# Optimization experiments

Measured on AMD Instinct MI355X. Metric: run time of the kernel, lower is better.

## Reference

```python
import jax, jax.numpy as jnp
import numpy as np

B, T = 256, 128
DW = 768          # dim_word
DH = 768          # dim_hidden (must equal DW per broadcast in original code)
NC = 3            # num_classification
VOCAB = 50000
TVOCAB = 5000


def setup_inputs() -> dict:
    key = jax.random.key(0)
    ks = jax.random.split(key, 16)
    u = 1.0 / np.sqrt(DH)
    uni = lambda k, shape: jax.random.uniform(k, shape, jnp.float32, -u, u)
    inp = {
        'sent': jax.random.randint(ks[0], (B, T), 0, VOCAB),
        'target': jax.random.randint(ks[1], (B,), 0, TVOCAB),
        'lens': jnp.clip(jax.random.randint(ks[2], (B,), 0, T + 1), 1, T),
        'emb': jax.random.normal(ks[3], (VOCAB, DW), jnp.float32) * 0.1,
        'temb': jax.random.normal(ks[4], (TVOCAB, DW), jnp.float32) * 0.1,
        # LSTM cell params: input = cat(x_t, target_x) -> 2*DW
        'W_ih': uni(ks[5], (2 * DW, 4 * DH)),
        'W_hh': uni(ks[6], (DH, 4 * DH)),
        'b_lstm': uni(ks[7], (4 * DH,)),
        'Wh': uni(ks[8], (DH, DH)),
        'Wv': uni(ks[9], (DW, DW)),
        'w': uni(ks[10], (DH + DW,)),
        'Wp': uni(ks[11], (DH, DH)),
        'Wx': uni(ks[12], (DH, DH)),
        'W_lin': uni(ks[13], (DH, NC)),
        'b_lin': uni(ks[14], (NC,)),
    }
    return inp


def _forward(sent, target, lens, emb, temb, W_ih, W_hh, b_lstm, Wh, Wv, w, Wp, Wx, W_lin, b_lin):
    x = emb[sent]                      # [B, T, DW]
    tx = temb[target]                  # [B, DW]
    mask = (jnp.arange(T)[None, :] < lens[:, None]).astype(x.dtype)  # [B, T]

    def step(carry, ins):
        h, c = carry
        xt, mt = ins                   # [B, DW], [B]
        inp = jnp.concatenate([xt, tx], axis=-1)          # [B, 2*DW]
        gates = inp @ W_ih + h @ W_hh + b_lstm            # [B, 4*DH]
        i, f, g, o = jnp.split(gates, 4, axis=-1)
        c_new = jax.nn.sigmoid(f) * c + jax.nn.sigmoid(i) * jnp.tanh(g)
        h_new = jax.nn.sigmoid(o) * jnp.tanh(c_new)
        m = mt[:, None]
        h = m * h_new + (1.0 - m) * h   # mask blend (hold state past seq end)
        c = m * c_new + (1.0 - m) * c
        return (h, c), h

    h0 = jnp.zeros((x.shape[0], DH), x.dtype)
    c0 = jnp.zeros((x.shape[0], DH), x.dtype)
    xs = (jnp.swapaxes(x, 0, 1), mask.T)                 # time-major
    _, Hs = jax.lax.scan(step, (h0, c0), xs)
    H = jnp.swapaxes(Hs, 0, 1)                            # [B, T, DH]

    # attention: M = tanh([H Wh ; aspect Wv]); scores = M @ w, masked softmax
    aspect_proj = (tx @ Wv)[:, None, :]                   # [B, 1, DW] broadcast over T
    M = jnp.tanh(jnp.concatenate(
        [H @ Wh, jnp.broadcast_to(aspect_proj, H.shape)], axis=-1))  # [B, T, DH+DW]
    scores = M @ w                                        # [B, T]
    scores = jnp.where(mask > 0, scores, -1e9)
    alpha = jax.nn.softmax(scores, axis=-1)               # [B, T]
    r = jnp.einsum('bt,btd->bd', alpha, H)                # [B, DH]
    h_star = jnp.tanh(r @ Wp + H[:, -1, :] @ Wx)          # [B, DH]
    # dropout is identity in eval mode
    logit = h_star @ W_lin + b_lin                        # [B, NC]
    return logit


def reference(sent, target, lens, emb, temb, W_ih, W_hh, b_lstm, Wh, Wv, w, Wp, Wx, W_lin, b_lin):
    return _forward(sent, target, lens, emb, temb, W_ih, W_hh, b_lstm,
                    Wh, Wv, w, Wp, Wx, W_lin, b_lin)
```

## Files before the change

kernel.cpp:

```cpp
#include <hip/hip_runtime.h>
#include <stdint.h>

#define Bz 256
#define Tz 128
#define DWz 768
#define DHz 768
#define G4z 3072
#define NBLK 96
#define NGRID 256

typedef __attribute__((ext_vector_type(8))) short short8;
typedef __attribute__((ext_vector_type(4))) float f32x4;
typedef __attribute__((ext_vector_type(4))) int i32x4;

__device__ __forceinline__ unsigned short f2bf(float x) {
    union { float f; unsigned int u; } v; v.f = x;
    unsigned int u = v.u;
    return (unsigned short)((u + 0x7fffu + ((u >> 16) & 1u)) >> 16);
}
__device__ __forceinline__ float bf2f(unsigned short h) {
    union { unsigned int u; float f; } v; v.u = ((unsigned int)h) << 16;
    return v.f;
}
__device__ __forceinline__ float fsigm(float x) {
// ... 175 lines not shown
    int s0 = tid, s1 = tid + 256;
    int bd0 = (s0 >> 2) * 40 + (((s0 & 3) ^ (((s0 >> 2) >> 3) & 3)) << 3);
    int bd1 = (s1 >> 2) * 40 + (((s1 & 3) ^ (((s1 >> 2) >> 3) & 3)) << 3);

    f32x4 acc[4][4];
    f32x4 zz = {0.f, 0.f, 0.f, 0.f};
#pragma unroll
    for (int i = 0; i < 4; ++i)
#pragma unroll
        for (int j = 0; j < 4; ++j) acc[i][j] = zz;

    for (int k0 = 0; k0 < DWz; k0 += 32) {
        {
            const float* src = emb + gbase + k0 + kp;
            alignas(16) unsigned short tmp[16];
#pragma unroll
            for (int it = 0; it < 4; ++it) {
                float4 v = ((const float4*)src)[it];
                tmp[it * 4 + 0] = f2bf(v.x); tmp[it * 4 + 1] = f2bf(v.y);
                tmp[it * 4 + 2] = f2bf(v.z); tmp[it * 4 + 3] = f2bf(v.w);
            }
            *(int4*)(sA + arow * 40 + kp) = *(const int4*)tmp;
            *(int4*)(sA + arow * 40 + kp + 8) = *(const int4*)(tmp + 8);
        }
        {
            const int4* wsrc = (const int4*)WbP
                + ((long)((k0 >> 5) * 24 + (n0 >> 7))) * 512 + tid;
            int4 v0 = wsrc[0];
            int4 v1 = wsrc[256];
            *(int4*)(sB + bd0) = v0;
            *(int4*)(sB + bd1) = v1;
        }
        __syncthreads();
        short8 af[4], bfr[4];
#pragma unroll
        for (int i = 0; i < 4; ++i)
            af[i] = *(const short8*)(sA + (wm * 64 + i * 16 + l15) * 40 + q * 8);
#pragma unroll
        for (int j = 0; j < 4; ++j) {
            int n = wn * 64 + j * 16 + l15;
            bfr[j] = *(const short8*)(sB + n * 40 + ((q ^ ((n >> 3) & 3)) << 3));
        }
#pragma unroll
        for (int i = 0; i < 4; ++i)
#pragma unroll
            for (int j = 0; j < 4; ++j)
                acc[i][j] = __builtin_amdgcn_mfma_f32_16x16x32_bf16(af[i], bfr[j], acc[i][j], 0, 0, 0);
        __syncthreads();
    }
#pragma unroll
    for (int j = 0; j < 4; ++j) {
        int n = n0 + wn * 64 + j * 16 + l15;
        int gt = n / 768;
        int dblk = (n - gt * 768) >> 4;
#pragma unroll
        for (int ip = 0; ip < 2; ++ip) {
            int row = m0 + wm * 64 + ip * 32;
            int t = row >> 8;
            int bq = (row & 255) + q * 4;
            int blk = dblk * 2 + (bq >> 7);
            int tidd = ((bq & 127) >> 5) * 64 + q * 16 + l15;
            alignas(16) unsigned short o[8];
#pragma unroll
            for (int r = 0; r < 4; ++r) {
                o[r]     = f2bf(acc[ip * 2][j][r]);
                o[4 + r] = f2bf(acc[ip * 2 + 1][j][r]);
            }
            *(int4*)(xW + (((long)t * 96 + blk) * 4 + gt) * 2048 + (long)tidd * 8) = *(const int4*)o;
        }
    }
}

#define UNPACK(PF, G)                                                        \
    {                                                                        \
        const unsigned short* ch_ = (const unsigned short*)&(PF);            \
        _Pragma("unroll")                                                    \
        for (int i_ = 0; i_ < 2; ++i_)                                       \
            _Pragma("unroll")                                                \
            for (int r_ = 0; r_ < 4; ++r_)                                   \
                xg[i_][G][r_] = bf2f(ch_[i_ * 4 + r_]) + xgc[i_][G][r_];     \
    }

__global__ __launch_bounds__(256, 1) void k_lstm_all(int t0, int t1,
        unsigned short* __restrict__ xW, const float* __restrict__ constg,
        const unsigned short* __restrict__ WhhP, unsigned short* __restrict__ Hbf,
        float* __restrict__ cbuf, const int* __restrict__ lens,
        unsigned* __restrict__ bar, unsigned* __restrict__ xwcnt, int waitxw,
        const float* __restrict__ emb, const int* __restrict__ sent,
        const unsigned short* __restrict__ WihbP, int nprod,
        const unsigned short* __restrict__ WhbP, const float* __restrict__ wv,
        float* __restrict__ scores) {
    extern __shared__ unsigned short sB[];
    int bid = blockIdx.x;
    int tid = threadIdx.x;
    int lane = tid & 63, wid = tid >> 6;
    int l15 = lane & 15, q = lane >> 4;

    if (bid >= NBLK) {
        unsigned short* psA = sB;
        unsigned short* psB = sB + 5120;
        float* sred = (float*)(sB + 10240);
        int wm = wid >> 1, wn = wid & 1;
        int arow = tid >> 1;
        int kp = (tid & 1) * 16;
        int s0 = tid, s1 = tid + 256;
        int bd0 = (s0 >> 2) * 40 + (((s0 & 3) ^ (((s0 >> 2) >> 3) & 3)) << 3);
        int bd1 = (s1 >> 2) * 40 + (((s1 & 3) ^ (((s1 >> 2) >> 3) & 3)) << 3);

        for (int g = bid - NBLK; g < 6144; g += nprod) {
            int my = g / 24, nx = g - (g / 24) * 24;
            int m0 = my * 128, n0 = nx * 128;
            int m = m0 + arow;
            int tt = m >> 8, bb2 = m & 255;
            long gbase = (long)sent[bb2 * Tz + tt] * DWz;

            f32x4 acc[4][4];
            f32x4 zz = {0.f, 0.f, 0.f, 0.f};
#pragma unroll
            for (int i = 0; i < 4; ++i)
#pragma unroll
                for (int j = 0; j < 4; ++j) acc[i][j] = zz;

            for (int k0 = 0; k0 < DWz; k0 += 32) {
                {
                    const float* src = emb + gbase + k0 + kp;
                    alignas(16) unsigned short tmp[16];
#pragma unroll
                    for (int it = 0; it < 4; ++it) {
                        float4 v = ((const float4*)src)[it];
                        tmp[it * 4 + 0] = f2bf(v.x); tmp[it * 4 + 1] = f2bf(v.y);
                        tmp[it * 4 + 2] = f2bf(v.z); tmp[it * 4 + 3] = f2bf(v.w);
                    }
                    *(int4*)(psA + arow * 40 + kp) = *(const int4*)tmp;
                    *(int4*)(psA + arow * 40 + kp + 8) = *(const int4*)(tmp + 8);
                }
                {
                    const int4* wsrc = (const int4*)WihbP
                        + ((long)((k0 >> 5) * 24 + (n0 >> 7))) * 512 + tid;
                    int4 v0 = wsrc[0];
                    int4 v1 = wsrc[256];
                    *(int4*)(psB + bd0) = v0;
                    *(int4*)(psB + bd1) = v1;
                }
                __syncthreads();
                short8 af[4], bfr[4];
#pragma unroll
                for (int i = 0; i < 4; ++i)
                    af[i] = *(const short8*)(psA + (wm * 64 + i * 16 + l15) * 40 + q * 8);
#pragma unroll
                for (int j = 0; j < 4; ++j) {
                    int n = wn * 64 + j * 16 + l15;
                    bfr[j] = *(const short8*)(psB + n * 40 + ((q ^ ((n >> 3) & 3)) << 3));
                }
#pragma unroll
                for (int i = 0; i < 4; ++i)
#pragma unroll
                    for (int j = 0; j < 4; ++j)
                        acc[i][j] = __builtin_amdgcn_mfma_f32_16x16x32_bf16(af[i], bfr[j], acc[i][j], 0, 0, 0);
                __syncthreads();
            }
#pragma unroll
            for (int j = 0; j < 4; ++j) {
                int n = n0 + wn * 64 + j * 16 + l15;
                int gt = n / 768;
                int dblk2 = (n - gt * 768) >> 4;
#pragma unroll
                for (int ip = 0; ip < 2; ++ip) {
                    int row = m0 + wm * 64 + ip * 32;
                    int t = row >> 8;
                    int bq = (row & 255) + q * 4;
                    int blk = dblk2 * 2 + (bq >> 7);
                    int tidd = ((bq & 127) >> 5) * 64 + q * 16 + l15;
                    alignas(16) unsigned short o[8];
#pragma unroll
                    for (int r = 0; r < 4; ++r) {
                        o[r]     = f2bf(acc[ip * 2][j][r]);
                        o[4 + r] = f2bf(acc[ip * 2 + 1][j][r]);
                    }
                    unsigned long long* dst = (unsigned long long*)
                        (xW + (((long)t * 96 + blk) * 4 + gt) * 2048 + (long)tidd * 8);
                    const unsigned long long* po = (const unsigned long long*)o;
                    __hip_atomic_store(dst, po[0], __ATOMIC_RELAXED, __HIP_MEMORY_SCOPE_AGENT);
                    __hip_atomic_store(dst + 1, po[1], __ATOMIC_RELAXED, __HIP_MEMORY_SCOPE_AGENT);
                }
            }
            asm volatile("s_waitcnt vmcnt(0)" ::: "memory");
            __syncthreads();
            if (tid == 0)
                (void)__hip_atomic_fetch_add(&xwcnt[(my >> 1) * 32], 1u,
                                             __ATOMIC_RELAXED, __HIP_MEMORY_SCOPE_AGENT);
        }

        for (int s2 = bid - NBLK; s2 < 1536; s2 += nprod) {
            int t = s2 / 12;
            int rr = s2 - t * 12;
            int mt = rr / 6, nt2 = rr - (rr / 6) * 6;
            int m0 = mt * 128, n0 = nt2 * 128;
            unsigned tgt = (unsigned)(t + 1);
            {
                const unsigned* fp2 = bar + (((mt * 4 + wid) * 48) + lane) * 32;
                while (true) {
                    unsigned v = (lane < 48)
                        ? __hip_atomic_load(fp2, __ATOMIC_RELAXED, __HIP_MEMORY_SCOPE_AGENT)
                        : tgt;
                    if (__all(v >= tgt)) break;
                    __builtin_amdgcn_s_sleep(8);
                }
            }
            __syncthreads();

            f32x4 acc[4][4];
            f32x4 zz = {0.f, 0.f, 0.f, 0.f};
#pragma unroll
            for (int i = 0; i < 4; ++i)
#pragma unroll
                for (int j = 0; j < 4; ++j) acc[i][j] = zz;

            for (int k0 = 0; k0 < DHz; k0 += 32) {
                {
                    const unsigned short* asrc = Hbf
                        + ((long)(m0 + arow) * Tz + t) * DHz + k0 + kp;
                    *(int4*)(psA + arow * 40 + kp) = *(const int4*)asrc;
                    *(int4*)(psA + arow * 40 + kp + 8) = *(const int4*)(asrc + 8);
                }
                {
                    const int4* wsrc = (const int4*)WhbP
                        + ((long)((k0 >> 5) * 6 + nt2)) * 512 + tid;
                    int4 v0 = wsrc[0];
                    int4 v1 = wsrc[256];
                    *(int4*)(psB + bd0) = v0;
                    *(int4*)(psB + bd1) = v1;
                }
                __syncthreads();
                short8 af[4], bfr[4];
#pragma unroll
                for (int i = 0; i < 4; ++i)
                    af[i] = *(const short8*)(psA + (wm * 64 + i * 16 + l15) * 40 + q * 8);
#pragma unroll
                for (int j = 0; j < 4; ++j) {
                    int n = wn * 64 + j * 16 + l15;
                    bfr[j] = *(const short8*)(psB + n * 40 + ((q ^ ((n >> 3) & 3)) << 3));
                }
#pragma unroll
                for (int i = 0; i < 4; ++i)
#pragma unroll
                    for (int j = 0; j < 4; ++j)
                        acc[i][j] = __builtin_amdgcn_mfma_f32_16x16x32_bf16(af[i], bfr[j], acc[i][j], 0, 0, 0);
                __syncthreads();
            }
            if (tid < 128) sred[tid] = 0.f;
            __syncthreads();
#pragma unroll
            for (int i = 0; i < 4; ++i)
#pragma unroll
                for (int r = 0; r < 4; ++r) {
                    float sv = 0.f;
#pragma unroll
                    for (int j = 0; j < 4; ++j) {
                        int n = n0 + wn * 64 + j * 16 + l15;
                        sv += ftanh(acc[i][j][r]) * wv[n];
                    }
#pragma unroll
                    for (int o = 1; o < 16; o <<= 1) sv += __shfl_xor(sv, o, 64);
                    if (l15 == 0) atomicAdd(&sred[wm * 64 + i * 16 + q * 4 + r], sv);
                }
            __syncthreads();
            if (tid < 128)
                atomicAdd(&scores[(long)(m0 + tid) * Tz + t], sred[tid]);
        }
        return;
    }

    int bm = bid & 1;
    int dblk = bid >> 1;
    int d0 = dblk * 16;
    int d = d0 + l15;
    unsigned* flg = bar + ((bm * 4 + wid) * 48) * 32;

    {
        const int4* src = (const int4*)WhhP + (long)dblk * 6144;
        for (int s = tid; s < 6144; s += 256) ((int4*)sB)[s] = src[s];
    }

    int brow[8];
    int lenr[8];
    float c[8], h[8];
    float xgc[2][4][4];
#pragma unroll
    for (int i = 0; i < 2; ++i)
#pragma unroll
        for (int r = 0; r < 4; ++r) {
            int ir = i * 4 + r;
            int b = bm * 128 + wid * 32 + i * 16 + q * 4 + r;
            brow[ir] = b;
            lenr[ir] = lens[b];
            long cbase = (long)b * G4z + d;
#pragma unroll
            for (int j = 0; j < 4; ++j) xgc[i][j][r] = constg[cbase + j * 768];
            if (t0 > 0) {
                c[ir] = cbuf[(long)b * DHz + d];
                h[ir] = bf2f(Hbf[((long)b * Tz + (t0 - 1)) * DHz + d]);
            } else { c[ir] = 0.f; h[ir] = 0.f; }
        }

    int bbase[4];
#pragma unroll
    for (int j = 0; j < 4; ++j) {
        int nl = j * 16 + l15;
        bbase[j] = nl * 32 + ((q ^ ((nl >> 1) & 3)) << 3);
    }
    __syncthreads();

    if (waitxw) {
        const unsigned* xc = xwcnt + t0 * 32;
        if (lane == 0)
            while (__hip_atomic_load(xc, __ATOMIC_RELAXED, __HIP_MEMORY_SCOPE_AGENT) < 48u)
                __builtin_amdgcn_s_sleep(1);
        asm volatile("" ::: "memory");
    }
    float xg[2][4][4];
    {
        const unsigned short* x0 = xW + ((long)t0 * 96 + bid) * 8192 + (long)tid * 8;
        int4 c0 = *(const int4*)(x0);
        int4 c1 = *(const int4*)(x0 + 2048);
        int4 c2 = *(const int4*)(x0 + 4096);
        int4 c3 = *(const int4*)(x0 + 6144);
        UNPACK(c0, 0) UNPACK(c1, 1) UNPACK(c2, 2) UNPACK(c3, 3)
    }

    i32x4 pf0, pf1, pf2, pf3;

    for (int t = t0; t < t1; ++t) {
        if (t > t0) {
            unsigned tgt = (unsigned)t;
            const unsigned* fp = flg + lane * 32;
            while (true) {
                unsigned v = (lane < 48)
                    ? __hip_atomic_load(fp, __ATOMIC_RELAXED, __HIP_MEMORY_SCOPE_AGENT)
                    : tgt;
                if (__all(v >= tgt)) break;
                __builtin_amdgcn_s_sleep(1);
            }
            asm volatile("s_waitcnt vmcnt(0)" ::: "memory");
            __builtin_amdgcn_sched_barrier(0);
            UNPACK(pf0, 0) UNPACK(pf1, 1) UNPACK(pf2, 2) UNPACK(pf3, 3)
        }

        f32x4 acc[2][4];
        f32x4 zz = {0.f, 0.f, 0.f, 0.f};
#pragma unroll
        for (int i = 0; i < 2; ++i)
#pragma unroll
            for (int j = 0; j < 4; ++j) acc[i][j] = zz;

        if (t > 0) {
            const unsigned short* ap0 = Hbf + ((long)(bm * 128 + wid * 32 + l15) * Tz + (t - 1)) * DHz + q * 8;
            const unsigned short* ap1 = ap0 + (long)16 * Tz * DHz;
#pragma unroll 6
            for (int k0c = 0; k0c < 24; ++k0c) {
                short8 a0 = *(const short8*)(ap0 + k0c * 32);
                short8 a1 = *(const short8*)(ap1 + k0c * 32);
                const unsigned short* bb = sB + k0c * 2048;
#pragma unroll
                for (int j = 0; j < 4; ++j) {
                    short8 bf = *(const short8*)(bb + bbase[j]);
                    acc[0][j] = __builtin_amdgcn_mfma_f32_16x16x32_bf16(a0, bf, acc[0][j], 0, 0, 0);
                    acc[1][j] = __builtin_amdgcn_mfma_f32_16x16x32_bf16(a1, bf, acc[1][j], 0, 0, 0);
                }
            }
        }

#pragma unroll
        for (int i = 0; i < 2; ++i)
#pragma unroll
            for (int r = 0; r < 4; ++r) {
                int ir = i * 4 + r;
                float gi = acc[i][0][r] + xg[i][0][r];
                float gf = acc[i][1][r] + xg[i][1][r];
                float gg = acc[i][2][r] + xg[i][2][r];
                float go = acc[i][3][r] + xg[i][3][r];
                float cn = fsigm(gf) * c[ir] + fsigm(gi) * ftanh(gg);
                float hn = fsigm(go) * ftanh(cn);
                bool upd = t < lenr[ir];
                c[ir] = upd ? cn : c[ir];
                h[ir] = upd ? hn : h[ir];
                __hip_atomic_store(Hbf + ((long)brow[ir] * Tz + t) * DHz + d, f2bf(h[ir]),
                                   __ATOMIC_RELAXED, __HIP_MEMORY_SCOPE_AGENT);
            }

        if (t + 1 < t1) {
            if (waitxw) {
                const unsigned* xc = xwcnt + (t + 1) * 32;
                if (lane == 0)
                    while (__hip_atomic_load(xc, __ATOMIC_RELAXED, __HIP_MEMORY_SCOPE_AGENT) < 48u)
                        __builtin_amdgcn_s_sleep(1);
                asm volatile("" ::: "memory");
            }
            const unsigned short* pp = xW + ((long)(t + 1) * 96 + bid) * 8192 + (long)tid * 8;
            asm volatile(
                "global_load_dwordx4 %0, %4, off\n\t"
                "global_load_dwordx4 %1, %5, off\n\t"
                "global_load_dwordx4 %2, %6, off\n\t"
                "global_load_dwordx4 %3, %7, off"
                : "=&v"(pf0), "=&v"(pf1), "=&v"(pf2), "=&v"(pf3)
                : "v"(pp), "v"(pp + 2048), "v"(pp + 4096), "v"(pp + 6144)
                : "memory");
            asm volatile("s_waitcnt vmcnt(4)" ::: "memory");
            if (lane == 0)
                __hip_atomic_store(flg + dblk * 32, (unsigned)(t + 1),
                                   __ATOMIC_RELAXED, __HIP_MEMORY_SCOPE_AGENT);
        }
    }
    asm volatile("s_waitcnt vmcnt(0)" ::: "memory");
    if (lane == 0)
        __hip_atomic_store(flg + dblk * 32, (unsigned)t1,
                           __ATOMIC_RELAXED, __HIP_MEMORY_SCOPE_AGENT);
#pragma unroll
    for (int ir = 0; ir < 8; ++ir) cbuf[(long)brow[ir] * DHz + d] = c[ir];
}

__global__ __launch_bounds__(256) void k_scores(const unsigned short* __restrict__ Hbf,
                                                const unsigned short* __restrict__ WbP,
                                                const float* __restrict__ wv,
                                                float* __restrict__ scores) {
    __shared__ unsigned short sA[128 * 40];
    __shared__ unsigned short sB[128 * 40];
    __shared__ float sred[128];
    int tid = threadIdx.x;
    int n0 = blockIdx.x * 128;
    int m0 = blockIdx.y * 128;
    int wid = tid >> 6, lane = tid & 63, l15 = lane & 15, q = lane >> 4;
    int wm = wid >> 1, wn = wid & 1;

    int s0 = tid, s1 = tid + 256;
    int bd0 = (s0 >> 2) * 40 + (((s0 & 3) ^ (((s0 >> 2) >> 3) & 3)) << 3);
    int bd1 = (s1 >> 2) * 40 + (((s1 & 3) ^ (((s1 >> 2) >> 3) & 3)) << 3);

    f32x4 acc[4][4];
    f32x4 zz = {0.f, 0.f, 0.f, 0.f};
#pragma unroll
    for (int i = 0; i < 4; ++i)
#pragma unroll
        for (int j = 0; j < 4; ++j) acc[i][j] = zz;

    int arow = tid >> 1;
    int kp = (tid & 1) * 16;
    const unsigned short* asrc = Hbf + (long)(m0 + arow) * DHz;

    for (int k0 = 0; k0 < DHz; k0 += 32) {
        *(int4*)(sA + arow * 40 + kp) = *(const int4*)(asrc + k0 + kp);
        *(int4*)(sA + arow * 40 + kp + 8) = *(const int4*)(asrc + k0 + kp + 8);
        {
            const int4* wsrc = (const int4*)WbP
                + ((long)((k0 >> 5) * 6 + (n0 >> 7))) * 512 + tid;
            int4 v0 = wsrc[0];
            int4 v1 = wsrc[256];
            *(int4*)(sB + bd0) = v0;
            *(int4*)(sB + bd1) = v1;
        }
        __syncthreads();
        short8 af[4], bfr[4];
#pragma unroll
        for (int i = 0; i < 4; ++i)
            af[i] = *(const short8*)(sA + (wm * 64 + i * 16 + l15) * 40 + q * 8);
#pragma unroll
        for (int j = 0; j < 4; ++j) {
            int n = wn * 64 + j * 16 + l15;
            bfr[j] = *(const short8*)(sB + n * 40 + ((q ^ ((n >> 3) & 3)) << 3));
        }
#pragma unroll
        for (int i = 0; i < 4; ++i)
#pragma unroll
            for (int j = 0; j < 4; ++j)
                acc[i][j] = __builtin_amdgcn_mfma_f32_16x16x32_bf16(af[i], bfr[j], acc[i][j], 0, 0, 0);
        __syncthreads();
    }
    if (tid < 128) sred[tid] = 0.f;
    __syncthreads();
#pragma unroll
    for (int i = 0; i < 4; ++i)
#pragma unroll
        for (int r = 0; r < 4; ++r) {
            float sv = 0.f;
#pragma unroll
            for (int j = 0; j < 4; ++j) {
                int n = n0 + wn * 64 + j * 16 + l15;
                sv += ftanh(acc[i][j][r]) * wv[n];
            }
#pragma unroll
            for (int o = 1; o < 16; o <<= 1) sv += __shfl_xor(sv, o, 64);
            if (l15 == 0) atomicAdd(&sred[wm * 64 + i * 16 + q * 4 + r], sv);
        }
    __syncthreads();
    if (tid < 128) atomicAdd(&scores[m0 + tid], sred[tid]);
}

__global__ __launch_bounds__(128) void k_attn(const float* __restrict__ scores,
                                              const int* __restrict__ lens,
                                              const unsigned short* __restrict__ Hbf,
                                              float* __restrict__ rbuf) {
    int b = blockIdx.x, t = threadIdx.x;
    __shared__ float sal[Tz];
    __shared__ float rA[2], rB[2];
    int len = lens[b];
    float s = (t < len) ? scores[b * Tz + t] : -1e9f;
    float m = s;
#pragma unroll
    for (int o = 32; o; o >>= 1) m = fmaxf(m, __shfl_xor(m, o, 64));
    if ((t & 63) == 0) rA[t >> 6] = m;
    __syncthreads();
    m = fmaxf(rA[0], rA[1]);
    float e = expf(s - m);
    float sum = e;
#pragma unroll
    for (int o = 32; o; o >>= 1) sum += __shfl_xor(sum, o, 64);
    if ((t & 63) == 0) rB[t >> 6] = sum;
    __syncthreads();
    sum = rB[0] + rB[1];
    sal[t] = e / sum;
    __syncthreads();
    if (t < 96) {
        const unsigned short* hp = Hbf + (long)b * Tz * DHz + t * 8;
        float acc[8] = {};
        for (int tt = 0; tt < Tz; ++tt) {
            short8 v = *(const short8*)(hp + (long)tt * DHz);
            float a = sal[tt];
            const unsigned short* pv = (const unsigned short*)&v;
#pragma unroll
            for (int e2 = 0; e2 < 8; ++e2) acc[e2] += a * bf2f(pv[e2]);
        }
        float* rp = rbuf + (long)b * DHz + t * 8;
#pragma unroll
        for (int e2 = 0; e2 < 8; ++e2) rp[e2] = acc[e2];
    }
}

__global__ __launch_bounds__(256) void k_hstar(const float* __restrict__ rbuf,
                                               const unsigned short* __restrict__ Hbf,
                                               const unsigned short* __restrict__ WbP,
                                               float* __restrict__ hst) {
    __shared__ unsigned short sA[128 * 40];
    __shared__ unsigned short sB[128 * 40];
    int tid = threadIdx.x;
    int n0 = blockIdx.x * 128;
    int m0 = blockIdx.y * 128;
    int wid = tid >> 6, lane = tid & 63, l15 = lane & 15, q = lane >> 4;
    int wm = wid >> 1, wn = wid & 1;
    int arow = tid >> 1;
    int kp = (tid & 1) * 16;
    int s0 = tid, s1 = tid + 256;
    int bd0 = (s0 >> 2) * 40 + (((s0 & 3) ^ (((s0 >> 2) >> 3) & 3)) << 3);
    int bd1 = (s1 >> 2) * 40 + (((s1 & 3) ^ (((s1 >> 2) >> 3) & 3)) << 3);

    f32x4 acc[4][4];
    f32x4 zz = {0.f, 0.f, 0.f, 0.f};
#pragma unroll
    for (int i = 0; i < 4; ++i)
#pragma unroll
        for (int j = 0; j < 4; ++j) acc[i][j] = zz;

    for (int k0 = 0; k0 < 2 * DHz; k0 += 32) {
        if (k0 < DHz) {
            const float* src = rbuf + (long)(m0 + arow) * DHz + k0 + kp;
            alignas(16) unsigned short tmp[16];
#pragma unroll
            for (int it = 0; it < 4; ++it) {
                float4 v = ((const float4*)src)[it];
                tmp[it * 4 + 0] = f2bf(v.x); tmp[it * 4 + 1] = f2bf(v.y);
                tmp[it * 4 + 2] = f2bf(v.z); tmp[it * 4 + 3] = f2bf(v.w);
            }
            *(int4*)(sA + arow * 40 + kp) = *(const int4*)tmp;
            *(int4*)(sA + arow * 40 + kp + 8) = *(const int4*)(tmp + 8);
        } else {
            const unsigned short* src = Hbf + ((long)(m0 + arow) * Tz + (Tz - 1)) * DHz
                                      + (k0 - DHz) + kp;
            *(int4*)(sA + arow * 40 + kp) = *(const int4*)src;
            *(int4*)(sA + arow * 40 + kp + 8) = *(const int4*)(src + 8);
        }
        {
            const int4* wsrc = (const int4*)WbP
                + ((long)((k0 >> 5) * 6 + (n0 >> 7))) * 512 + tid;
            int4 v0 = wsrc[0];
            int4 v1 = wsrc[256];
            *(int4*)(sB + bd0) = v0;
            *(int4*)(sB + bd1) = v1;
        }
        __syncthreads();
        short8 af[4], bfr[4];
#pragma unroll
        for (int i = 0; i < 4; ++i)
            af[i] = *(const short8*)(sA + (wm * 64 + i * 16 + l15) * 40 + q * 8);
#pragma unroll
        for (int j = 0; j < 4; ++j) {
            int n = wn * 64 + j * 16 + l15;
            bfr[j] = *(const short8*)(sB + n * 40 + ((q ^ ((n >> 3) & 3)) << 3));
        }
#pragma unroll
        for (int i = 0; i < 4; ++i)
#pragma unroll
            for (int j = 0; j < 4; ++j)
                acc[i][j] = __builtin_amdgcn_mfma_f32_16x16x32_bf16(af[i], bfr[j], acc[i][j], 0, 0, 0);
        __syncthreads();
    }
#pragma unroll
    for (int i = 0; i < 4; ++i)
#pragma unroll
        for (int j = 0; j < 4; ++j) {
            int col = n0 + wn * 64 + j * 16 + l15;
#pragma unroll
            for (int r = 0; r < 4; ++r) {
                int row = m0 + wm * 64 + i * 16 + q * 4 + r;
                hst[(long)row * DHz + col] = ftanh(acc[i][j][r]);
            }
        }
}

__global__ void k_logits(const float* __restrict__ hst, const float* __restrict__ Wl,
                         const float* __restrict__ bl, float* __restrict__ out) {
    int b = blockIdx.x;
    int lane = threadIdx.x & 63, c = threadIdx.x >> 6;
    float s = 0.f;
    for (int k = lane; k < DHz; k += 64) s += hst[(long)b * DHz + k] * Wl[k * 3 + c];
#pragma unroll
    for (int o = 32; o; o >>= 1) s += __shfl_xor(s, o, 64);
    if (lane == 0) out[b * 3 + c] = s + bl[c];
}

extern "C" void kernel_launch(void* const* d_in, const int* in_sizes, int n_in,
                              void* d_out, int out_size, void* d_ws, size_t ws_size,
                              hipStream_t stream) {
    (void)in_sizes; (void)n_in; (void)out_size; (void)ws_size;
    const int*   sent   = (const int*)d_in[0];
    const int*   target = (const int*)d_in[1];
    const int*   lens   = (const int*)d_in[2];
    const float* emb    = (const float*)d_in[3];
    const float* temb   = (const float*)d_in[4];
    const float* W_ih   = (const float*)d_in[5];
    const float* W_hh   = (const float*)d_in[6];
    const float* b_lstm = (const float*)d_in[7];
    const float* Wh     = (const float*)d_in[8];
    const float* wv     = (const float*)d_in[10];
    const float* Wp     = (const float*)d_in[11];
    const float* Wx     = (const float*)d_in[12];
    const float* W_lin  = (const float*)d_in[13];
    const float* b_lin  = (const float*)d_in[14];
    float* out = (float*)d_out;

    char* ws = (char*)d_ws;
    size_t off = 0;
    auto alloc = [&](size_t bytes) -> void* {
        void* p = ws + off;
        off = (off + bytes + 255) & ~(size_t)255;
        return p;
    };
    unsigned short* xW    = (unsigned short*)alloc((size_t)32768 * G4z * 2);
    unsigned short* Hbf   = (unsigned short*)alloc((size_t)Bz * Tz * DHz * 2);
    unsigned short* WihbP = (unsigned short*)alloc((size_t)24 * 24 * 512 * 16);
    unsigned short* Wih2P = (unsigned short*)alloc((size_t)24 * 24 * 512 * 16);
    unsigned short* WhhP  = (unsigned short*)alloc((size_t)48 * 6144 * 16);
    unsigned short* WhbP  = (unsigned short*)alloc((size_t)24 * 6 * 512 * 16);
    unsigned short* WpxP  = (unsigned short*)alloc((size_t)48 * 6 * 512 * 16);
    float* constg = (float*)alloc((size_t)Bz * G4z * 4);
    float* cbuf   = (float*)alloc((size_t)Bz * DHz * 4);
    float* scores = (float*)alloc((size_t)Bz * Tz * 4);
    float* rbuf   = (float*)alloc((size_t)Bz * DHz * 4);
    float* hst    = (float*)alloc((size_t)Bz * DHz * 4);
    unsigned* bar = (unsigned*)alloc(65536);
    unsigned* xwc = (unsigned*)alloc(16384);

    k_prep_all<<<1584, 256, 0, stream>>>(W_ih, Wh, Wp, Wx, WihbP, Wih2P, WhbP, WpxP);
    k_prep_whh<<<1152, 256, 0, stream>>>(W_hh, WhhP);
    hipMemsetAsync(scores, 0, (size_t)Bz * Tz * 4, stream);
    hipMemsetAsync(bar, 0, 65536, stream);
    hipMemsetAsync(xwc, 0, 16384, stream);

    k_gemm_cg<<<dim3(24, 2), 256, 0, stream>>>(target, temb, Wih2P, b_lstm, constg);

    hipFuncSetAttribute((const void*)k_lstm_all,
                        hipFuncAttributeMaxDynamicSharedMemorySize, 98304);
    int t0v = 0, t1v = Tz, waitv = 1, nprodv = NGRID - NBLK;
    unsigned short* xWp = xW;
    const float* cgp = constg;
    const unsigned short* whp = WhhP;
    unsigned short* hbp = Hbf;
    float* cbp = cbuf;
    const int* lnp = lens;
    unsigned* barp = bar;
    unsigned* xwcp = xwc;
    const float* embp = emb;
    const int* sentp = sent;
    const unsigned short* wihp = WihbP;
    const unsigned short* whbp = WhbP;
    const float* wvp = wv;
    float* scp = scores;
    void* kargs[] = {&t0v, &t1v, &xWp, &cgp, &whp, &hbp, &cbp, &lnp, &barp,
                     &xwcp, &waitv, &embp, &sentp, &wihp, &nprodv,
                     &whbp, &wvp, &scp};
    hipError_t ce = hipLaunchCooperativeKernel(reinterpret_cast<void*>(k_lstm_all),
                                               dim3(NGRID), dim3(256), kargs, 98304, stream);
    if (ce != hipSuccess) {
        k_gemm_x<<<dim3(24, 256), 256, 0, stream>>>(emb, sent, WihbP, xW);
        for (int t = 0; t < Tz; ++t)
            k_lstm_all<<<NBLK, 256, 98304, stream>>>(t, t + 1, xW, constg, WhhP, Hbf,
                                                     cbuf, lens, bar, xwc, 0,
                                                     emb, sent, WihbP, 0,
                                                     WhbP, wv, scores);
        k_scores<<<dim3(6, 256), 256, 0, stream>>>(Hbf, WhbP, wv, scores);
    }

    k_attn<<<Bz, 128, 0, stream>>>(scores, lens, Hbf, rbuf);
    k_hstar<<<dim3(6, 2), 256, 0, stream>>>(rbuf, Hbf, WpxP, hst);
    k_logits<<<Bz, 192, 0, stream>>>(hst, W_lin, b_lin, out);
}
```

Before: 1.858 ms.

## Fuse constant-gate GEMM and attention epilogue into the persistent cooperative LSTM kernel

Moves the target-embedding gate GEMM (constg) into the producer blocks of the persistent cooperative kernel, with LSTM blocks spinning on a counter before they read it. The attention softmax, h_star GEMM and logits also move into the same kernel as tasks gated by global atomic counters. This removes the separate launches and their serialization gaps before and after the recurrent loop. In exchange it adds spin-waits and more kernel arguments and registers, and relies on every block being co-resident.

```diff
diff --git a/kernel.cpp b/kernel.cpp
--- a/kernel.cpp
+++ b/kernel.cpp
@@ -281,19 +281,25 @@
     }
 
 __global__ __launch_bounds__(256, 1) void k_lstm_all(int t0, int t1,
-        unsigned short* __restrict__ xW, const float* __restrict__ constg,
+        unsigned short* __restrict__ xW, float* __restrict__ constg,
         const unsigned short* __restrict__ WhhP, unsigned short* __restrict__ Hbf,
         float* __restrict__ cbuf, const int* __restrict__ lens,
-        unsigned* __restrict__ bar, unsigned* __restrict__ xwcnt, int waitxw,
+        unsigned* __restrict__ bar, unsigned* __restrict__ xwcnt, int fused,
         const float* __restrict__ emb, const int* __restrict__ sent,
         const unsigned short* __restrict__ WihbP, int nprod,
         const unsigned short* __restrict__ WhbP, const float* __restrict__ wv,
-        float* __restrict__ scores) {
+        float* __restrict__ scores,
+        const int* __restrict__ target, const float* __restrict__ temb,
+        const unsigned short* __restrict__ Wih2P, const float* __restrict__ b_lstm,
+        float* __restrict__ rbuf, const unsigned short* __restrict__ WpxP,
+        float* __restrict__ hst, const float* __restrict__ W_lin,
+        const float* __restrict__ b_lin, float* __restrict__ out) {
     extern __shared__ unsigned short sB[];
     int bid = blockIdx.x;
     int tid = threadIdx.x;
     int lane = tid & 63, wid = tid >> 6;
     int l15 = lane & 15, q = lane >> 4;
+    unsigned* ctr = bar + 12288;
 
     if (bid >= NBLK) {
         unsigned short* psA = sB;
@@ -305,6 +311,75 @@
         int s0 = tid, s1 = tid + 256;
         int bd0 = (s0 >> 2) * 40 + (((s0 & 3) ^ (((s0 >> 2) >> 3) & 3)) << 3);
         int bd1 = (s1 >> 2) * 40 + (((s1 & 3) ^ (((s1 >> 2) >> 3) & 3)) << 3);
+
+        for (int cg = bid - NBLK; cg < 48; cg += nprod) {
+            int my = cg / 24, nx = cg - my * 24;
+            int m0 = my * 128, n0 = nx * 128;
+            long gbase = (long)target[m0 + arow] * DWz;
+            f32x4 acc[4][4];
+            f32x4 zz = {0.f, 0.f, 0.f, 0.f};
+#pragma unroll
+            for (int i = 0; i < 4; ++i)
+#pragma unroll
+                for (int j = 0; j < 4; ++j) acc[i][j] = zz;
+            for (int k0 = 0; k0 < DWz; k0 += 32) {
+                {
+                    const float* src = temb + gbase + k0 + kp;
+                    alignas(16) unsigned short tmp[16];
+#pragma unroll
+                    for (int it = 0; it < 4; ++it) {
+                        float4 v = ((const float4*)src)[it];
+                        tmp[it * 4 + 0] = f2bf(v.x); tmp[it * 4 + 1] = f2bf(v.y);
+                        tmp[it * 4 + 2] = f2bf(v.z); tmp[it * 4 + 3] = f2bf(v.w);
+                    }
+                    *(int4*)(psA + arow * 40 + kp) = *(const int4*)tmp;
+                    *(int4*)(psA + arow * 40 + kp + 8) = *(const int4*)(tmp + 8);
+                }
+                {
+                    const int4* wsrc = (const int4*)Wih2P
+                        + ((long)((k0 >> 5) * 24 + (n0 >> 7))) * 512 + tid;
+                    int4 v0 = wsrc[0];
+                    int4 v1 = wsrc[256];
+                    *(int4*)(psB + bd0) = v0;
+                    *(int4*)(psB + bd1) = v1;
+                }
+                __syncthreads();
+                short8 af[4], bfr[4];
+#pragma unroll
+                for (int i = 0; i < 4; ++i)
+                    af[i] = *(const short8*)(psA + (wm * 64 + i * 16 + l15) * 40 + q * 8);
+#pragma unroll
+                for (int j = 0; j < 4; ++j) {
+                    int n = wn * 64 + j * 16 + l15;
+                    bfr[j] = *(const short8*)(psB + n * 40 + ((q ^ ((n >> 3) & 3)) << 3));
+                }
+#pragma unroll
+                for (int i = 0; i < 4; ++i)
+#pragma unroll
+                    for (int j = 0; j < 4; ++j)
+                        acc[i][j] = __builtin_amdgcn_mfma_f32_16x16x32_bf16(af[i], bfr[j], acc[i][j], 0, 0, 0);
+                __syncthreads();
+            }
+#pragma unroll
+            for (int i = 0; i < 4; ++i)
+#pragma unroll
+                for (int j = 0; j < 4; ++j) {
+                    int col = n0 + wn * 64 + j * 16 + l15;
+                    float bv = b_lstm[col];
+#pragma unroll
+                    for (int r = 0; r < 4; ++r) {
+                        int row = m0 + wm * 64 + i * 16 + q * 4 + r;
+                        __hip_atomic_store(&constg[(long)row * G4z + col],
+                                           acc[i][j][r] + bv,
+                                           __ATOMIC_RELAXED, __HIP_MEMORY_SCOPE_AGENT);
+                    }
+                }
+            asm volatile("s_waitcnt vmcnt(0)" ::: "memory");
+            __syncthreads();
+            if (tid == 0)
+                (void)__hip_atomic_fetch_add(ctr, 1u, __ATOMIC_RELAXED,
+                                             __HIP_MEMORY_SCOPE_AGENT);
+        }
 
         for (int g = bid - NBLK; g < 6144; g += nprod) {
             int my = g / 24, nx = g - (g / 24) * 24;
@@ -466,156 +541,333 @@
             __syncthreads();
             if (tid < 128)
                 atomicAdd(&scores[(long)(m0 + tid) * Tz + t], sred[tid]);
-        }
-        return;
-    }
-
-    int bm = bid & 1;
-    int dblk = bid >> 1;
-    int d0 = dblk * 16;
-    int d = d0 + l15;
-    unsigned* flg = bar + ((bm * 4 + wid) * 48) * 32;
-
-    {
-        const int4* src = (const int4*)WhhP + (long)dblk * 6144;
-        for (int s = tid; s < 6144; s += 256) ((int4*)sB)[s] = src[s];
-    }
-
-    int brow[8];
-    int lenr[8];
-    float c[8], h[8];
-    float xgc[2][4][4];
-#pragma unroll
-    for (int i = 0; i < 2; ++i)
-#pragma unroll
-        for (int r = 0; r < 4; ++r) {
-            int ir = i * 4 + r;
-            int b = bm * 128 + wid * 32 + i * 16 + q * 4 + r;
-            brow[ir] = b;
-            lenr[ir] = lens[b];
-            long cbase = (long)b * G4z + d;
-#pragma unroll
-            for (int j = 0; j < 4; ++j) xgc[i][j][r] = constg[cbase + j * 768];
-            if (t0 > 0) {
-                c[ir] = cbuf[(long)b * DHz + d];
-                h[ir] = bf2f(Hbf[((long)b * Tz + (t0 - 1)) * DHz + d]);
-            } else { c[ir] = 0.f; h[ir] = 0.f; }
-        }
-
-    int bbase[4];
-#pragma unroll
-    for (int j = 0; j < 4; ++j) {
-        int nl = j * 16 + l15;
-        bbase[j] = nl * 32 + ((q ^ ((nl >> 1) & 3)) << 3);
-    }
-    __syncthreads();
-
-    if (waitxw) {
-        const unsigned* xc = xwcnt + t0 * 32;
-        if (lane == 0)
-            while (__hip_atomic_load(xc, __ATOMIC_RELAXED, __HIP_MEMORY_SCOPE_AGENT) < 48u)
-                __builtin_amdgcn_s_sleep(1);
-        asm volatile("" ::: "memory");
-    }
-    float xg[2][4][4];
-    {
-        const unsigned short* x0 = xW + ((long)t0 * 96 + bid) * 8192 + (long)tid * 8;
-        int4 c0 = *(const int4*)(x0);
-        int4 c1 = *(const int4*)(x0 + 2048);
-        int4 c2 = *(const int4*)(x0 + 4096);
-        int4 c3 = *(const int4*)(x0 + 6144);
-        UNPACK(c0, 0) UNPACK(c1, 1) UNPACK(c2, 2) UNPACK(c3, 3)
-    }
-
-    i32x4 pf0, pf1, pf2, pf3;
-
-    for (int t = t0; t < t1; ++t) {
-        if (t > t0) {
-            unsigned tgt = (unsigned)t;
-            const unsigned* fp = flg + lane * 32;
-            while (true) {
-                unsigned v = (lane < 48)
-                    ? __hip_atomic_load(fp, __ATOMIC_RELAXED, __HIP_MEMORY_SCOPE_AGENT)
-                    : tgt;
-                if (__all(v >= tgt)) break;
-                __builtin_amdgcn_s_sleep(1);
-            }
             asm volatile("s_waitcnt vmcnt(0)" ::: "memory");
-            __builtin_amdgcn_sched_barrier(0);
-            UNPACK(pf0, 0) UNPACK(pf1, 1) UNPACK(pf2, 2) UNPACK(pf3, 3)
-        }
-
-        f32x4 acc[2][4];
-        f32x4 zz = {0.f, 0.f, 0.f, 0.f};
-#pragma unroll
-        for (int i = 0; i < 2; ++i)
-#pragma unroll
-            for (int j = 0; j < 4; ++j) acc[i][j] = zz;
-
-        if (t > 0) {
-            const unsigned short* ap0 = Hbf + ((long)(bm * 128 + wid * 32 + l15) * Tz + (t - 1)) * DHz + q * 8;
-            const unsigned short* ap1 = ap0 + (long)16 * Tz * DHz;
-#pragma unroll 6
-            for (int k0c = 0; k0c < 24; ++k0c) {
-                short8 a0 = *(const short8*)(ap0 + k0c * 32);
-                short8 a1 = *(const short8*)(ap1 + k0c * 32);
-                const unsigned short* bb = sB + k0c * 2048;
-#pragma unroll
-                for (int j = 0; j < 4; ++j) {
-                    short8 bf = *(const short8*)(bb + bbase[j]);
-                    acc[0][j] = __builtin_amdgcn_mfma_f32_16x16x32_bf16(a0, bf, acc[0][j], 0, 0, 0);
-                    acc[1][j] = __builtin_amdgcn_mfma_f32_16x16x32_bf16(a1, bf, acc[1][j], 0, 0, 0);
-                }
-            }
-        }
-
+            __syncthreads();
+            if (tid == 0)
+                (void)__hip_atomic_fetch_add(ctr + 32, 1u, __ATOMIC_RELAXED,
+                                             __HIP_MEMORY_SCOPE_AGENT);
+        }
+    } else {
+        int bm = bid & 1;
+        int dblk = bid >> 1;
+        int d0 = dblk * 16;
+        int d = d0 + l15;
+        unsigned* flg = bar + ((bm * 4 + wid) * 48) * 32;
+
+        {
+            const int4* src = (const int4*)WhhP + (long)dblk * 6144;
+            for (int s = tid; s < 6144; s += 256) ((int4*)sB)[s] = src[s];
+        }
+
+        int brow[8];
+        int lenr[8];
+        float c[8], h[8];
 #pragma unroll
         for (int i = 0; i < 2; ++i)
 #pragma unroll
             for (int r = 0; r < 4; ++r) {
                 int ir = i * 4 + r;
-                float gi = acc[i][0][r] + xg[i][0][r];
-                float gf = acc[i][1][r] + xg[i][1][r];
-                float gg = acc[i][2][r] + xg[i][2][r];
-                float go = acc[i][3][r] + xg[i][3][r];
-                float cn = fsigm(gf) * c[ir] + fsigm(gi) * ftanh(gg);
-                float hn = fsigm(go) * ftanh(cn);
-                bool upd = t < lenr[ir];
-                c[ir] = upd ? cn : c[ir];
-                h[ir] = upd ? hn : h[ir];
-                __hip_atomic_store(Hbf + ((long)brow[ir] * Tz + t) * DHz + d, f2bf(h[ir]),
-                                   __ATOMIC_RELAXED, __HIP_MEMORY_SCOPE_AGENT);
-            }
-
-        if (t + 1 < t1) {
-            if (waitxw) {
-                const unsigned* xc = xwcnt + (t + 1) * 32;
+                int b = bm * 128 + wid * 32 + i * 16 + q * 4 + r;
+                brow[ir] = b;
+                lenr[ir] = lens[b];
+                if (t0 > 0) {
+                    c[ir] = cbuf[(long)b * DHz + d];
+                    h[ir] = bf2f(Hbf[((long)b * Tz + (t0 - 1)) * DHz + d]);
+                } else { c[ir] = 0.f; h[ir] = 0.f; }
+            }
+
+        int bbase[4];
+#pragma unroll
+        for (int j = 0; j < 4; ++j) {
+            int nl = j * 16 + l15;
+            bbase[j] = nl * 32 + ((q ^ ((nl >> 1) & 3)) << 3);
+        }
+        if (fused && tid == 0)
+            while (__hip_atomic_load(ctr, __ATOMIC_RELAXED, __HIP_MEMORY_SCOPE_AGENT) < 48u)
+                __builtin_amdgcn_s_sleep(1);
+        __syncthreads();
+
+        float xgc[2][4][4];
+#pragma unroll
+        for (int i = 0; i < 2; ++i)
+#pragma unroll
+            for (int r = 0; r < 4; ++r) {
+                long cbase = (long)brow[i * 4 + r] * G4z + d;
+#pragma unroll
+                for (int j = 0; j < 4; ++j) xgc[i][j][r] = constg[cbase + j * 768];
+            }
+
+        if (fused) {
+            const unsigned* xc = xwcnt + t0 * 32;
+            if (lane == 0)
+                while (__hip_atomic_load(xc, __ATOMIC_RELAXED, __HIP_MEMORY_SCOPE_AGENT) < 48u)
+                    __builtin_amdgcn_s_sleep(1);
+            asm volatile("" ::: "memory");
+        }
+        float xg[2][4][4];
+        {
+            const unsigned short* x0 = xW + ((long)t0 * 96 + bid) * 8192 + (long)tid * 8;
+            int4 c0 = *(const int4*)(x0);
+            int4 c1 = *(const int4*)(x0 + 2048);
+            int4 c2 = *(const int4*)(x0 + 4096);
+            int4 c3 = *(const int4*)(x0 + 6144);
+            UNPACK(c0, 0) UNPACK(c1, 1) UNPACK(c2, 2) UNPACK(c3, 3)
+        }
+
+        i32x4 pf0, pf1, pf2, pf3;
+
+        for (int t = t0; t < t1; ++t) {
+            if (t > t0) {
+                unsigned tgt = (unsigned)t;
+                const unsigned* fp = flg + lane * 32;
+                while (true) {
+                    unsigned v = (lane < 48)
+                        ? __hip_atomic_load(fp, __ATOMIC_RELAXED, __HIP_MEMORY_SCOPE_AGENT)
+                        : tgt;
+                    if (__all(v >= tgt)) break;
+                    __builtin_amdgcn_s_sleep(1);
+                }
+                asm volatile("s_waitcnt vmcnt(0)" ::: "memory");
+                __builtin_amdgcn_sched_barrier(0);
+                UNPACK(pf0, 0) UNPACK(pf1, 1) UNPACK(pf2, 2) UNPACK(pf3, 3)
+            }
+
+            f32x4 acc[2][4];
+            f32x4 zz = {0.f, 0.f, 0.f, 0.f};
+#pragma unroll
+            for (int i = 0; i < 2; ++i)
+#pragma unroll
+                for (int j = 0; j < 4; ++j) acc[i][j] = zz;
+
+            if (t > 0) {
+                const unsigned short* ap0 = Hbf + ((long)(bm * 128 + wid * 32 + l15) * Tz + (t - 1)) * DHz + q * 8;
+                const unsigned short* ap1 = ap0 + (long)16 * Tz * DHz;
+#pragma unroll 6
+                for (int k0c = 0; k0c < 24; ++k0c) {
+                    short8 a0 = *(const short8*)(ap0 + k0c * 32);
+                    short8 a1 = *(const short8*)(ap1 + k0c * 32);
+                    const unsigned short* bb = sB + k0c * 2048;
+#pragma unroll
+                    for (int j = 0; j < 4; ++j) {
+                        short8 bf = *(const short8*)(bb + bbase[j]);
+                        acc[0][j] = __builtin_amdgcn_mfma_f32_16x16x32_bf16(a0, bf, acc[0][j], 0, 0, 0);
+                        acc[1][j] = __builtin_amdgcn_mfma_f32_16x16x32_bf16(a1, bf, acc[1][j], 0, 0, 0);
+                    }
+                }
+            }
+
+#pragma unroll
+            for (int i = 0; i < 2; ++i)
+#pragma unroll
+                for (int r = 0; r < 4; ++r) {
+                    int ir = i * 4 + r;
+                    float gi = acc[i][0][r] + xg[i][0][r];
+                    float gf = acc[i][1][r] + xg[i][1][r];
+                    float gg = acc[i][2][r] + xg[i][2][r];
+                    float go = acc[i][3][r] + xg[i][3][r];
+                    float cn = fsigm(gf) * c[ir] + fsigm(gi) * ftanh(gg);
+                    float hn = fsigm(go) * ftanh(cn);
+                    bool upd = t < lenr[ir];
+                    c[ir] = upd ? cn : c[ir];
+                    h[ir] = upd ? hn : h[ir];
+                    __hip_atomic_store(Hbf + ((long)brow[ir] * Tz + t) * DHz + d, f2bf(h[ir]),
+                                       __ATOMIC_RELAXED, __HIP_MEMORY_SCOPE_AGENT);
+                }
+
+            if (t + 1 < t1) {
+                if (fused) {
+                    const unsigned* xc = xwcnt + (t + 1) * 32;
+                    if (lane == 0)
+                        while (__hip_atomic_load(xc, __ATOMIC_RELAXED, __HIP_MEMORY_SCOPE_AGENT) < 48u)
+                            __builtin_amdgcn_s_sleep(1);
+                    asm volatile("" ::: "memory");
+                }
+                const unsigned short* pp = xW + ((long)(t + 1) * 96 + bid) * 8192 + (long)tid * 8;
+                asm volatile(
+                    "global_load_dwordx4 %0, %4, off\n\t"
+                    "global_load_dwordx4 %1, %5, off\n\t"
+                    "global_load_dwordx4 %2, %6, off\n\t"
+                    "global_load_dwordx4 %3, %7, off"
+                    : "=&v"(pf0), "=&v"(pf1), "=&v"(pf2), "=&v"(pf3)
+                    : "v"(pp), "v"(pp + 2048), "v"(pp + 4096), "v"(pp + 6144)
+                    : "memory");
+                asm volatile("s_waitcnt vmcnt(4)" ::: "memory");
                 if (lane == 0)
-                    while (__hip_atomic_load(xc, __ATOMIC_RELAXED, __HIP_MEMORY_SCOPE_AGENT) < 48u)
-                        __builtin_amdgcn_s_sleep(1);
-                asm volatile("" ::: "memory");
-            }
-            const unsigned short* pp = xW + ((long)(t + 1) * 96 + bid) * 8192 + (long)tid * 8;
-            asm volatile(
-                "global_load_dwordx4 %0, %4, off\n\t"
-                "global_load_dwordx4 %1, %5, off\n\t"
-                "global_load_dwordx4 %2, %6, off\n\t"
-                "global_load_dwordx4 %3, %7, off"
-                : "=&v"(pf0), "=&v"(pf1), "=&v"(pf2), "=&v"(pf3)
-                : "v"(pp), "v"(pp + 2048), "v"(pp + 4096), "v"(pp + 6144)
-                : "memory");
-            asm volatile("s_waitcnt vmcnt(4)" ::: "memory");
-            if (lane == 0)
-                __hip_atomic_store(flg + dblk * 32, (unsigned)(t + 1),
-                                   __ATOMIC_RELAXED, __HIP_MEMORY_SCOPE_AGENT);
-        }
-    }
-    asm volatile("s_waitcnt vmcnt(0)" ::: "memory");
-    if (lane == 0)
-        __hip_atomic_store(flg + dblk * 32, (unsigned)t1,
-                           __ATOMIC_RELAXED, __HIP_MEMORY_SCOPE_AGENT);
-#pragma unroll
-    for (int ir = 0; ir < 8; ++ir) cbuf[(long)brow[ir] * DHz + d] = c[ir];
+                    __hip_atomic_store(flg + dblk * 32, (unsigned)(t + 1),
+                                       __ATOMIC_RELAXED, __HIP_MEMORY_SCOPE_AGENT);
+            }
+        }
+        asm volatile("s_waitcnt vmcnt(0)" ::: "memory");
+        if (lane == 0)
+            __hip_atomic_store(flg + dblk * 32, (unsigned)t1,
+                               __ATOMIC_RELAXED, __HIP_MEMORY_SCOPE_AGENT);
+#pragma unroll
+        for (int ir = 0; ir < 8; ++ir) cbuf[(long)brow[ir] * DHz + d] = c[ir];
+    }
+
+    if (!fused) return;
+
+    __syncthreads();
+    {
+        unsigned short* eA = sB;
+        unsigned short* eB = sB + 5120;
+        float* esal = (float*)(sB + 10240);
+        float* erAB = esal + 128;
+        int wm = wid >> 1, wn = wid & 1;
+        int arow = tid >> 1;
+        int kp = (tid & 1) * 16;
+        int s0 = tid, s1 = tid + 256;
+        int bd0 = (s0 >> 2) * 40 + (((s0 & 3) ^ (((s0 >> 2) >> 3) & 3)) << 3);
+        int bd1 = (s1 >> 2) * 40 + (((s1 & 3) ^ (((s1 >> 2) >> 3) & 3)) << 3);
+
+        for (int task = bid; task < 524; task += NGRID) {
+            if (task < 256) {
+                int b = task;
+                if (tid == 0)
+                    while (__hip_atomic_load(ctr + 32, __ATOMIC_RELAXED,
+                                             __HIP_MEMORY_SCOPE_AGENT) < 1536u)
+                        __builtin_amdgcn_s_sleep(8);
+                __syncthreads();
+                float e = 0.f, mm = 0.f, sv = 0.f;
+                if (tid < 128) {
+                    int len = lens[b];
+                    sv = (tid < len) ? scores[b * Tz + tid] : -1e9f;
+                    mm = sv;
+#pragma unroll
+                    for (int o = 32; o; o >>= 1) mm = fmaxf(mm, __shfl_xor(mm, o, 64));
+                    if ((tid & 63) == 0) erAB[tid >> 6] = mm;
+                }
+                __syncthreads();
+                if (tid < 128) {
+                    mm = fmaxf(erAB[0], erAB[1]);
+                    e = expf(sv - mm);
+                    float sum = e;
+#pragma unroll
+                    for (int o = 32; o; o >>= 1) sum += __shfl_xor(sum, o, 64);
+                    if ((tid & 63) == 0) erAB[2 + (tid >> 6)] = sum;
+                }
+                __syncthreads();
+                if (tid < 128) esal[tid] = e / (erAB[2] + erAB[3]);
+                __syncthreads();
+                if (tid < 96) {
+                    const unsigned short* hp = Hbf + (long)b * Tz * DHz + tid * 8;
+                    float acc8[8] = {};
+                    for (int tt = 0; tt < Tz; ++tt) {
+                        short8 v = *(const short8*)(hp + (long)tt * DHz);
+                        float a = esal[tt];
+                        const unsigned short* pv = (const unsigned short*)&v;
+#pragma unroll
+                        for (int e2 = 0; e2 < 8; ++e2) acc8[e2] += a * bf2f(pv[e2]);
+                    }
+                    float* rp = rbuf + (long)b * DHz + tid * 8;
+#pragma unroll
+                    for (int e2 = 0; e2 < 8; e2 += 2) {
+                        union { float f[2]; unsigned long long u; } pk;
+                        pk.f[0] = acc8[e2]; pk.f[1] = acc8[e2 + 1];
+                        __hip_atomic_store((unsigned long long*)(rp + e2), pk.u,
+                                           __ATOMIC_RELAXED, __HIP_MEMORY_SCOPE_AGENT);
+                    }
+                }
+                asm volatile("s_waitcnt vmcnt(0)" ::: "memory");
+                __syncthreads();
+                if (tid == 0)
+                    (void)__hip_atomic_fetch_add(ctr + 64, 1u, __ATOMIC_RELAXED,
+                                                 __HIP_MEMORY_SCOPE_AGENT);
+            } else if (task < 268) {
+                int tile = task - 256;
+                int mt = tile / 6, nt2 = tile - mt * 6;
+                int m0 = mt * 128, n0 = nt2 * 128;
+                if (tid == 0)
+                    while (__hip_atomic_load(ctr + 64, __ATOMIC_RELAXED,
+                                             __HIP_MEMORY_SCOPE_AGENT) < 256u)
+                        __builtin_amdgcn_s_sleep(8);
+                __syncthreads();
+                f32x4 acc[4][4];
+                f32x4 zz = {0.f, 0.f, 0.f, 0.f};
+#pragma unroll
+                for (int i = 0; i < 4; ++i)
+#pragma unroll
+                    for (int j = 0; j < 4; ++j) acc[i][j] = zz;
+                for (int k0 = 0; k0 < 2 * DHz; k0 += 32) {
+                    if (k0 < DHz) {
+                        const float* src = rbuf + (long)(m0 + arow) * DHz + k0 + kp;
+                        alignas(16) unsigned short tmp[16];
+#pragma unroll
+                        for (int it = 0; it < 4; ++it) {
+                            float4 v = ((const float4*)src)[it];
+                            tmp[it * 4 + 0] = f2bf(v.x); tmp[it * 4 + 1] = f2bf(v.y);
+                            tmp[it * 4 + 2] = f2bf(v.z); tmp[it * 4 + 3] = f2bf(v.w);
+                        }
+                        *(int4*)(eA + arow * 40 + kp) = *(const int4*)tmp;
+                        *(int4*)(eA + arow * 40 + kp + 8) = *(const int4*)(tmp + 8);
+                    } else {
+                        const unsigned short* src = Hbf
+                            + ((long)(m0 + arow) * Tz + (Tz - 1)) * DHz + (k0 - DHz) + kp;
+                        *(int4*)(eA + arow * 40 + kp) = *(const int4*)src;
+                        *(int4*)(eA + arow * 40 + kp + 8) = *(const int4*)(src + 8);
+                    }
+                    {
+                        const int4* wsrc = (const int4*)WpxP
+                            + ((long)((k0 >> 5) * 6 + nt2)) * 512 + tid;
+                        int4 v0 = wsrc[0];
+                        int4 v1 = wsrc[256];
+                        *(int4*)(eB + bd0) = v0;
+                        *(int4*)(eB + bd1) = v1;
+                    }
+                    __syncthreads();
+                    short8 af[4], bfr[4];
+#pragma unroll
+                    for (int i = 0; i < 4; ++i)
+                        af[i] = *(const short8*)(eA + (wm * 64 + i * 16 + l15) * 40 + q * 8);
+#pragma unroll
+                    for (int j = 0; j < 4; ++j) {
+                        int n = wn * 64 + j * 16 + l15;
+                        bfr[j] = *(const short8*)(eB + n * 40 + ((q ^ ((n >> 3) & 3)) << 3));
+                    }
+#pragma unroll
+                    for (int i = 0; i < 4; ++i)
+#pragma unroll
+                        for (int j = 0; j < 4; ++j)
+                            acc[i][j] = __builtin_amdgcn_mfma_f32_16x16x32_bf16(af[i], bfr[j], acc[i][j], 0, 0, 0);
+                    __syncthreads();
+                }
+#pragma unroll
+                for (int i = 0; i < 4; ++i)
+#pragma unroll
+                    for (int j = 0; j < 4; ++j) {
+                        int col = n0 + wn * 64 + j * 16 + l15;
+#pragma unroll
+                        for (int r = 0; r < 4; ++r) {
+                            int row = m0 + wm * 64 + i * 16 + q * 4 + r;
+                            __hip_atomic_store(&hst[(long)row * DHz + col],
+                                               ftanh(acc[i][j][r]),
+                                               __ATOMIC_RELAXED, __HIP_MEMORY_SCOPE_AGENT);
+                        }
+                    }
+                asm volatile("s_waitcnt vmcnt(0)" ::: "memory");
+                __syncthreads();
+                if (tid == 0)
+                    (void)__hip_atomic_fetch_add(ctr + 96, 1u, __ATOMIC_RELAXED,
+                                                 __HIP_MEMORY_SCOPE_AGENT);
+            } else {
+                int b = task - 268;
+                if (tid == 0)
+                    while (__hip_atomic_load(ctr + 96, __ATOMIC_RELAXED,
+                                             __HIP_MEMORY_SCOPE_AGENT) < 12u)
+                        __builtin_amdgcn_s_sleep(8);
+                __syncthreads();
+                if (tid < 192) {
+                    int ln = tid & 63, cc2 = tid >> 6;
+                    float s2 = 0.f;
+                    for (int k = ln; k < DHz; k += 64)
+                        s2 += hst[(long)b * DHz + k] * W_lin[k * 3 + cc2];
+#pragma unroll
+                    for (int o = 32; o; o >>= 1) s2 += __shfl_xor(s2, o, 64);
+                    if (ln == 0) out[b * 3 + cc2] = s2 + b_lin[cc2];
+                }
+            }
+        }
+    }
 }
 
 __global__ __launch_bounds__(256) void k_scores(const unsigned short* __restrict__ Hbf,
@@ -630,28 +882,23 @@
     int m0 = blockIdx.y * 128;
     int wid = tid >> 6, lane = tid & 63, l15 = lane & 15, q = lane >> 4;
     int wm = wid >> 1, wn = wid & 1;
-
     int s0 = tid, s1 = tid + 256;
     int bd0 = (s0 >> 2) * 40 + (((s0 & 3) ^ (((s0 >> 2) >> 3) & 3)) << 3);
     int bd1 = (s1 >> 2) * 40 + (((s1 & 3) ^ (((s1 >> 2) >> 3) & 3)) << 3);
-
     f32x4 acc[4][4];
     f32x4 zz = {0.f, 0.f, 0.f, 0.f};
 #pragma unroll
     for (int i = 0; i < 4; ++i)
 #pragma unroll
         for (int j = 0; j < 4; ++j) acc[i][j] = zz;
-
     int arow = tid >> 1;
     int kp = (tid & 1) * 16;
     const unsigned short* asrc = Hbf + (long)(m0 + arow) * DHz;
-
     for (int k0 = 0; k0 < DHz; k0 += 32) {
         *(int4*)(sA + arow * 40 + kp) = *(const int4*)(asrc + k0 + kp);
         *(int4*)(sA + arow * 40 + kp + 8) = *(const int4*)(asrc + k0 + kp + 8);
         {
-            const int4* wsrc = (const int4*)WbP
-                + ((long)((k0 >> 5) * 6 + (n0 >> 7))) * 512 + tid;
+            const int4* wsrc = (const int4*)WbP + ((long)((k0 >> 5) * 6 + (n0 >> 7))) * 512 + tid;
             int4 v0 = wsrc[0];
             int4 v1 = wsrc[256];
             *(int4*)(sB + bd0) = v0;
@@ -750,14 +997,12 @@
     int s0 = tid, s1 = tid + 256;
     int bd0 = (s0 >> 2) * 40 + (((s0 & 3) ^ (((s0 >> 2) >> 3) & 3)) << 3);
     int bd1 = (s1 >> 2) * 40 + (((s1 & 3) ^ (((s1 >> 2) >> 3) & 3)) << 3);
-
     f32x4 acc[4][4];
     f32x4 zz = {0.f, 0.f, 0.f, 0.f};
 #pragma unroll
     for (int i = 0; i < 4; ++i)
 #pragma unroll
         for (int j = 0; j < 4; ++j) acc[i][j] = zz;
-
     for (int k0 = 0; k0 < 2 * DHz; k0 += 32) {
         if (k0 < DHz) {
             const float* src = rbuf + (long)(m0 + arow) * DHz + k0 + kp;
@@ -777,8 +1022,7 @@
             *(int4*)(sA + arow * 40 + kp + 8) = *(const int4*)(src + 8);
         }
         {
-            const int4* wsrc = (const int4*)WbP
-                + ((long)((k0 >> 5) * 6 + (n0 >> 7))) * 512 + tid;
+            const int4* wsrc = (const int4*)WbP + ((long)((k0 >> 5) * 6 + (n0 >> 7))) * 512 + tid;
             int4 v0 = wsrc[0];
             int4 v1 = wsrc[256];
             *(int4*)(sB + bd0) = v0;
@@ -873,13 +1117,11 @@
     hipMemsetAsync(bar, 0, 65536, stream);
     hipMemsetAsync(xwc, 0, 16384, stream);
 
-    k_gemm_cg<<<dim3(24, 2), 256, 0, stream>>>(target, temb, Wih2P, b_lstm, constg);
-
     hipFuncSetAttribute((const void*)k_lstm_all,
                         hipFuncAttributeMaxDynamicSharedMemorySize, 98304);
-    int t0v = 0, t1v = Tz, waitv = 1, nprodv = NGRID - NBLK;
+    int t0v = 0, t1v = Tz, fusev = 1, nprodv = NGRID - NBLK;
     unsigned short* xWp = xW;
-    const float* cgp = constg;
+    float* cgp = constg;
     const unsigned short* whp = WhhP;
     unsigned short* hbp = Hbf;
     float* cbp = cbuf;
@@ -892,22 +1134,35 @@
     const unsigned short* whbp = WhbP;
     const float* wvp = wv;
     float* scp = scores;
+    const int* tgtp = target;
+    const float* tembp = temb;
+    const unsigned short* wih2p = Wih2P;
+    const float* blp = b_lstm;
+    float* rbp = rbuf;
+    const unsigned short* wpxp = WpxP;
+    float* hstp = hst;
+    const float* wlp = W_lin;
+    const float* blnp = b_lin;
+    float* outp = out;
     void* kargs[] = {&t0v, &t1v, &xWp, &cgp, &whp, &hbp, &cbp, &lnp, &barp,
-                     &xwcp, &waitv, &embp, &sentp, &wihp, &nprodv,
-                     &whbp, &wvp, &scp};
+                     &xwcp, &fusev, &embp, &sentp, &wihp, &nprodv,
+                     &whbp, &wvp, &scp, &tgtp, &tembp, &wih2p, &blp,
+                     &rbp, &wpxp, &hstp, &wlp, &blnp, &outp};
     hipError_t ce = hipLaunchCooperativeKernel(reinterpret_cast<void*>(k_lstm_all),
                                                dim3(NGRID), dim3(256), kargs, 98304, stream);
     if (ce != hipSuccess) {
+        k_gemm_cg<<<dim3(24, 2), 256, 0, stream>>>(target, temb, Wih2P, b_lstm, constg);
         k_gemm_x<<<dim3(24, 256), 256, 0, stream>>>(emb, sent, WihbP, xW);
         for (int t = 0; t < Tz; ++t)
             k_lstm_all<<<NBLK, 256, 98304, stream>>>(t, t + 1, xW, constg, WhhP, Hbf,
                                                      cbuf, lens, bar, xwc, 0,
                                                      emb, sent, WihbP, 0,
-                                                     WhbP, wv, scores);
+                                                     WhbP, wv, scores,
+                                                     target, temb, Wih2P, b_lstm,
+                                                     rbuf, WpxP, hst, W_lin, b_lin, out);
         k_scores<<<dim3(6, 256), 256, 0, stream>>>(Hbf, WhbP, wv, scores);
-    }
-
-    k_attn<<<Bz, 128, 0, stream>>>(scores, lens, Hbf, rbuf);
-    k_hstar<<<dim3(6, 2), 256, 0, stream>>>(rbuf, Hbf, WpxP, hst);
-    k_logits<<<Bz, 192, 0, stream>>>(hst, W_lin, b_lin, out);
-}
+        k_attn<<<Bz, 128, 0, stream>>>(scores, lens, Hbf, rbuf);
+        k_hstar<<<dim3(6, 2), 256, 0, stream>>>(rbuf, Hbf, WpxP, hst);
+        k_logits<<<Bz, 192, 0, stream>>>(hst, W_lin, b_lin, out);
+    }
+}
```

New measurement: 1.872 ms. No clear change (+0.8%).
